# Kernel optimization log

Hardware: AMD Instinct MI355X
Metric: run time of the kernel (lower is better)

The kernel has to match this reference:

```python
import jax, jax.numpy as jnp
import numpy as np
import itertools

# ResamplerLayer(interpolation='LINEAR', boundary='REPLICATE'): trilinear
# resampling with replicate (clamp-to-edge) boundary handling.
# inputs: [B, X, Y, Z, C]; sample_coords: [B, D0, D1, D2, 3] in voxel units.

B, X, Y, Z, C = 2, 128, 128, 128, 4
D = 96  # output grid size per spatial dim


def setup_inputs() -> dict:
    key = jax.random.key(0)
    k1, k2 = jax.random.split(key)
    inputs = jax.random.normal(k1, (B, X, Y, Z, C), dtype=jnp.float32)
    sizes = jnp.array([X, Y, Z], dtype=jnp.float32)
    # coordinates in [-1, size] to exercise the replicate boundary slightly
    sample_coords = jax.random.uniform(k2, (B, D, D, D, 3), dtype=jnp.float32) * (sizes + 1.0) - 1.0
    return {"inputs": inputs, "sample_coords": sample_coords}


def _trilinear_replicate(inputs, sample_coords):
    spatial = inputs.shape[1:-1]          # (X, Y, Z)
    bsz = inputs.shape[0]
    floor_c = jnp.floor(sample_coords)
    w = sample_coords - floor_c           # fractional weights, [B, D0, D1, D2, 3]
    base = floor_c.astype(jnp.int32)
    # batch index broadcast against the spatial coord grid
    b_idx = jnp.arange(bsz).reshape((bsz,) + (1,) * (sample_coords.ndim - 2))
    out = jnp.zeros(sample_coords.shape[:-1] + (inputs.shape[-1],), dtype=inputs.dtype)
    for bits in itertools.product((0, 1), repeat=3):  # 8 corners (binary neighbour ids)
        ix = jnp.clip(base[..., 0] + bits[0], 0, spatial[0] - 1)  # REPLICATE boundary
        iy = jnp.clip(base[..., 1] + bits[1], 0, spatial[1] - 1)
        iz = jnp.clip(base[..., 2] + bits[2], 0, spatial[2] - 1)
        vals = inputs[b_idx, ix, iy, iz]  # gather: [B, D0, D1, D2, C]
        weight = jnp.ones(sample_coords.shape[:-1], dtype=inputs.dtype)
        for d, bit in enumerate(bits):
            weight = weight * (w[..., d] if bit else (1.0 - w[..., d]))
        out = out + vals * weight[..., None]
    return out


def reference(inputs, sample_coords):
    return _trilinear_replicate(inputs, sample_coords)
```

## Files before the change

kernel.cpp:

```cpp
#include <hip/hip_runtime.h>
#include <hip/hip_fp16.h>

#define BATCH 2
#define NS 128
#define NB 64
#define ND 96

constexpr int PPB   = ND * ND * ND;
constexpr int TOTAL = BATCH * PPB;
constexpr int BRICKS_PER_BATCH = NB * NB * NB;
constexpr int TOTAL_BRICKS = BATCH * BRICKS_PER_BATCH;
constexpr size_t WS_NEEDED = (size_t)TOTAL_BRICKS * 64;

__device__ __forceinline__ float4 f4_lerp(float4 a, float4 b, float t) {
    float4 r;
    r.x = fmaf(b.x - a.x, t, a.x);
    r.y = fmaf(b.y - a.y, t, a.y);
    r.z = fmaf(b.z - a.z, t, a.z);
    r.w = fmaf(b.w - a.w, t, a.w);
    return r;
}

__global__ __launch_bounds__(256) void repack_fp16_bricks(
    const float4* __restrict__ in, uint2* __restrict__ bricks)
{
    int g = blockIdx.x * 256 + threadIdx.x;
    int t = g >> 3;
    int l = g & 7;
    int lx = (l >> 2) & 1, ly = (l >> 1) & 1, lz = l & 1;
    int b  = t >> 18;
    int r  = t & 262143;
    int x  = ((r >> 12) << 1) + lx;
    int y  = (((r >> 6) & 63) << 1) + ly;
    int z  = ((r & 63) << 1) + lz;

    float4 v = in[(((size_t)b * NS + x) * NS + y) * NS + z];
    __half2 h0 = __float22half2_rn(make_float2(v.x, v.y));
    __half2 h1 = __float22half2_rn(make_float2(v.z, v.w));
    uint2 p;
    p.x = *(const unsigned int*)&h0;
    p.y = *(const unsigned int*)&h1;
    bricks[g] = p;
}

__device__ __forceinline__ float4 vox_to_f4(uint2 v) {
    __half2 a = *(const __half2*)&v.x;
    __half2 b = *(const __half2*)&v.y;
    float2 f0 = __half22float2(a);
    float2 f1 = __half22float2(b);
    return make_float4(f0.x, f0.y, f1.x, f1.y);
}

__device__ __forceinline__ int brick_off(int x, int y, int z) {
    int bidx = (((x >> 1) * NB) + (y >> 1)) * NB + (z >> 1);
    return (bidx << 3) + ((x & 1) << 2) + ((y & 1) << 1) + (z & 1);
}

__global__ __launch_bounds__(256) void resample_bricks(
    const uint2* __restrict__ bricks,
    const float* __restrict__ coords,
    float4*      __restrict__ out)
{
    int idx = blockIdx.x * 256 + threadIdx.x;
    if (idx >= TOTAL) return;

    const float cx = coords[3 * idx + 0];
    const float cy = coords[3 * idx + 1];
    const float cz = coords[3 * idx + 2];

    const float fx = floorf(cx), fy = floorf(cy), fz = floorf(cz);
    const float wx = cx - fx, wy = cy - fy, wz = cz - fz;

    int x0 = max(0, min((int)fx,     NS - 1));
    int x1 = max(0, min((int)fx + 1, NS - 1));
    int y0 = max(0, min((int)fy,     NS - 1));
    int y1 = max(0, min((int)fy + 1, NS - 1));
    int z0 = max(0, min((int)fz,     NS - 1));
    int z1 = max(0, min((int)fz + 1, NS - 1));

    const uint2* __restrict__ wb =
        bricks + ((idx >= PPB) ? (size_t)BRICKS_PER_BATCH * 8 : 0);

    uint2 u000 = wb[brick_off(x0, y0, z0)];
    uint2 u001 = wb[brick_off(x0, y0, z1)];
    uint2 u010 = wb[brick_off(x0, y1, z0)];
    uint2 u011 = wb[brick_off(x0, y1, z1)];
    uint2 u100 = wb[brick_off(x1, y0, z0)];
    uint2 u101 = wb[brick_off(x1, y0, z1)];
    uint2 u110 = wb[brick_off(x1, y1, z0)];
    uint2 u111 = wb[brick_off(x1, y1, z1)];

    float4 c00 = f4_lerp(vox_to_f4(u000), vox_to_f4(u001), wz);
    float4 c01 = f4_lerp(vox_to_f4(u010), vox_to_f4(u011), wz);
    float4 c10 = f4_lerp(vox_to_f4(u100), vox_to_f4(u101), wz);
    float4 c11 = f4_lerp(vox_to_f4(u110), vox_to_f4(u111), wz);

    float4 c0 = f4_lerp(c00, c01, wy);
    float4 c1 = f4_lerp(c10, c11, wy);
    out[idx] = f4_lerp(c0, c1, wx);
}

__global__ __launch_bounds__(256) void resample_direct(
    const float4* __restrict__ in,
    const float*  __restrict__ coords,
    float4*       __restrict__ out)
{
    int idx = blockIdx.x * blockDim.x + threadIdx.x;
    if (idx >= TOTAL) return;

    const float cx = coords[3 * idx + 0];
    const float cy = coords[3 * idx + 1];
    const float cz = coords[3 * idx + 2];
    const float fx = floorf(cx), fy = floorf(cy), fz = floorf(cz);
    const float wx = cx - fx, wy = cy - fy, wz = cz - fz;

    int x0 = max(0, min((int)fx,     NS - 1));
    int x1 = max(0, min((int)fx + 1, NS - 1));
    int y0 = max(0, min((int)fy,     NS - 1));
    int y1 = max(0, min((int)fy + 1, NS - 1));
    int z0 = max(0, min((int)fz,     NS - 1));
    int z1 = max(0, min((int)fz + 1, NS - 1));

    const int b = idx / PPB;
    const float4* __restrict__ inb = in + (size_t)b * (NS * NS * NS);
    const float4* r00 = inb + ((size_t)x0 * NS + y0) * NS;
    const float4* r01 = inb + ((size_t)x0 * NS + y1) * NS;
    const float4* r10 = inb + ((size_t)x1 * NS + y0) * NS;
    const float4* r11 = inb + ((size_t)x1 * NS + y1) * NS;

    float4 c00 = f4_lerp(r00[z0], r00[z1], wz);
    float4 c01 = f4_lerp(r01[z0], r01[z1], wz);
    float4 c10 = f4_lerp(r10[z0], r10[z1], wz);
    float4 c11 = f4_lerp(r11[z0], r11[z1], wz);
    float4 c0 = f4_lerp(c00, c01, wy);
    float4 c1 = f4_lerp(c10, c11, wy);
    out[idx] = f4_lerp(c0, c1, wx);
}

extern "C" void kernel_launch(void* const* d_in, const int* in_sizes, int n_in,
                              void* d_out, int out_size, void* d_ws, size_t ws_size,
                              hipStream_t stream) {
    const float4* in     = (const float4*)d_in[0];
    const float*  coords = (const float*)d_in[1];
    float4*       out    = (float4*)d_out;

    if (ws_size >= WS_NEEDED) {
        uint2* bricks = (uint2*)d_ws;
        int rp_threads = TOTAL_BRICKS * 8;
        repack_fp16_bricks<<<rp_threads / 256, 256, 0, stream>>>(in, bricks);
        resample_bricks<<<(TOTAL + 255) / 256, 256, 0, stream>>>(bricks, coords, out);
    } else {
        resample_direct<<<(TOTAL + 255) / 256, 256, 0, stream>>>(in, coords, out);
    }
}
```

Before: 195.4 us.

## Build fp16 yz-neighbour table so each sample needs two 32-byte loads

Adds a precompute kernel that stores, for every voxel, the four fp16 (y,z) neighbour corners in one 32-byte entry, laid out with x innermost. Each trilinear sample then needs two contiguous 32-byte reads instead of eight scattered 8-byte gathers. Each thread handles one point from each batch and writes outputs with nontemporal stores. The cost is a 4x redundant table (128 MB of workspace and a larger precompute write), and boundary weights are clamped by hand so the replicate padding stays correct.

```diff
diff --git a/kernel.cpp b/kernel.cpp
--- a/kernel.cpp
+++ b/kernel.cpp
@@ -10,7 +10,11 @@
 constexpr int TOTAL = BATCH * PPB;
 constexpr int BRICKS_PER_BATCH = NB * NB * NB;
 constexpr int TOTAL_BRICKS = BATCH * BRICKS_PER_BATCH;
-constexpr size_t WS_NEEDED = (size_t)TOTAL_BRICKS * 64;
+constexpr size_t WS_BRICKS = (size_t)TOTAL_BRICKS * 64;
+constexpr int ENTRIES_PER_BATCH = NS * NS * NS;
+constexpr size_t WS_R4 = (size_t)BATCH * ENTRIES_PER_BATCH * 32;
+
+typedef float fx4 __attribute__((ext_vector_type(4)));
 
 __device__ __forceinline__ float4 f4_lerp(float4 a, float4 b, float t) {
     float4 r;
@@ -21,8 +25,113 @@
     return r;
 }
 
+__device__ __forceinline__ uint2 pack_h4(float4 v) {
+    __half2 h0 = __float22half2_rn(make_float2(v.x, v.y));
+    __half2 h1 = __float22half2_rn(make_float2(v.z, v.w));
+    uint2 p;
+    p.x = *(const unsigned int*)&h0;
+    p.y = *(const unsigned int*)&h1;
+    return p;
+}
+
+__device__ __forceinline__ float4 unpack_h4(unsigned int a, unsigned int b) {
+    float2 f0 = __half22float2(*(const __half2*)&a);
+    float2 f1 = __half22float2(*(const __half2*)&b);
+    return make_float4(f0.x, f0.y, f1.x, f1.y);
+}
+
+__global__ __launch_bounds__(256) void build_r4_table(
+    const fx4* __restrict__ in, uint4* __restrict__ tab)
+{
+    int g = blockIdx.x * 256 + threadIdx.x;
+    int b = g >> 21;
+    int r = g & ((1 << 21) - 1);
+    int x = r & 127;
+    int z = (r >> 7) & 127;
+    int y = r >> 14;
+    int y1 = min(y + 1, NS - 1);
+    int z1 = min(z + 1, NS - 1);
+
+    const fx4* __restrict__ row = in + (((size_t)b * NS + x) * NS) * NS;
+    fx4 v00 = row[(size_t)y  * NS + z ];
+    fx4 v01 = row[(size_t)y  * NS + z1];
+    fx4 v10 = row[(size_t)y1 * NS + z ];
+    fx4 v11 = row[(size_t)y1 * NS + z1];
+
+    uint2 p00 = pack_h4(make_float4(v00.x, v00.y, v00.z, v00.w));
+    uint2 p01 = pack_h4(make_float4(v01.x, v01.y, v01.z, v01.w));
+    uint2 p10 = pack_h4(make_float4(v10.x, v10.y, v10.z, v10.w));
+    uint2 p11 = pack_h4(make_float4(v11.x, v11.y, v11.z, v11.w));
+
+    tab[2 * g + 0] = make_uint4(p00.x, p00.y, p01.x, p01.y);
+    tab[2 * g + 1] = make_uint4(p10.x, p10.y, p11.x, p11.y);
+}
+
+__device__ __forceinline__ float4 sample_r4(
+    const uint4* __restrict__ tb, float cx, float cy, float cz)
+{
+    const float fx = floorf(cx), fy = floorf(cy), fz = floorf(cz);
+    const float wx = cx - fx;
+    const float wy = (fy < 0.f) ? 0.f : (cy - fy);
+    const float wz = (fz < 0.f) ? 0.f : (cz - fz);
+
+    int x0 = max(0, min((int)fx,     NS - 1));
+    int x1 = max(0, min((int)fx + 1, NS - 1));
+    int y0 = max(0, min((int)fy,     NS - 1));
+    int z0 = max(0, min((int)fz,     NS - 1));
+
+    int ebase = ((y0 << 7) + z0) << 7;
+    const uint4* e0 = tb + 2 * (ebase + x0);
+    const uint4* e1 = tb + 2 * (ebase + x1);
+
+    uint4 lo0 = e0[0], hi0 = e0[1];
+    uint4 lo1 = e1[0], hi1 = e1[1];
+
+    float4 a00 = unpack_h4(lo0.x, lo0.y), a01 = unpack_h4(lo0.z, lo0.w);
+    float4 a10 = unpack_h4(hi0.x, hi0.y), a11 = unpack_h4(hi0.z, hi0.w);
+    float4 b00 = unpack_h4(lo1.x, lo1.y), b01 = unpack_h4(lo1.z, lo1.w);
+    float4 b10 = unpack_h4(hi1.x, hi1.y), b11 = unpack_h4(hi1.z, hi1.w);
+
+    float4 cA0 = f4_lerp(a00, a01, wz);
+    float4 cA1 = f4_lerp(a10, a11, wz);
+    float4 cB0 = f4_lerp(b00, b01, wz);
+    float4 cB1 = f4_lerp(b10, b11, wz);
+    float4 cA  = f4_lerp(cA0, cA1, wy);
+    float4 cB  = f4_lerp(cB0, cB1, wy);
+    return f4_lerp(cA, cB, wx);
+}
+
+__device__ __forceinline__ void nt_store4(float4 v, fx4* p) {
+    fx4 t; t.x = v.x; t.y = v.y; t.z = v.z; t.w = v.w;
+    __builtin_nontemporal_store(t, p);
+}
+
+__global__ __launch_bounds__(256) void resample_r4(
+    const uint4* __restrict__ tab,
+    const float* __restrict__ coords,
+    fx4*         __restrict__ out)
+{
+    int idx = blockIdx.x * 256 + threadIdx.x;
+    const int idxB = idx + PPB;
+
+    const float axc = coords[3 * idx + 0];
+    const float ayc = coords[3 * idx + 1];
+    const float azc = coords[3 * idx + 2];
+    const float bxc = coords[3 * idxB + 0];
+    const float byc = coords[3 * idxB + 1];
+    const float bzc = coords[3 * idxB + 2];
+
+    const uint4* tb0 = tab;
+    const uint4* tb1 = tab + (size_t)ENTRIES_PER_BATCH * 2;
+
+    float4 rA = sample_r4(tb0, axc, ayc, azc);
+    float4 rB = sample_r4(tb1, bxc, byc, bzc);
+    nt_store4(rA, &out[idx]);
+    nt_store4(rB, &out[idxB]);
+}
+
 __global__ __launch_bounds__(256) void repack_fp16_bricks(
-    const float4* __restrict__ in, uint2* __restrict__ bricks)
+    const fx4* __restrict__ in, uint2* __restrict__ bricks)
 {
     int g = blockIdx.x * 256 + threadIdx.x;
     int t = g >> 3;
@@ -34,21 +143,12 @@
     int y  = (((r >> 6) & 63) << 1) + ly;
     int z  = ((r & 63) << 1) + lz;
 
-    float4 v = in[(((size_t)b * NS + x) * NS + y) * NS + z];
-    __half2 h0 = __float22half2_rn(make_float2(v.x, v.y));
-    __half2 h1 = __float22half2_rn(make_float2(v.z, v.w));
-    uint2 p;
-    p.x = *(const unsigned int*)&h0;
-    p.y = *(const unsigned int*)&h1;
-    bricks[g] = p;
+    fx4 v = __builtin_nontemporal_load(&in[(((size_t)b * NS + x) * NS + y) * NS + z]);
+    bricks[g] = pack_h4(make_float4(v.x, v.y, v.z, v.w));
 }
 
 __device__ __forceinline__ float4 vox_to_f4(uint2 v) {
-    __half2 a = *(const __half2*)&v.x;
-    __half2 b = *(const __half2*)&v.y;
-    float2 f0 = __half22float2(a);
-    float2 f1 = __half22float2(b);
-    return make_float4(f0.x, f0.y, f1.x, f1.y);
+    return unpack_h4(v.x, v.y);
 }
 
 __device__ __forceinline__ int brick_off(int x, int y, int z) {
@@ -67,7 +167,6 @@
     const float cx = coords[3 * idx + 0];
     const float cy = coords[3 * idx + 1];
     const float cz = coords[3 * idx + 2];
-
     const float fx = floorf(cx), fy = floorf(cy), fz = floorf(cz);
     const float wx = cx - fx, wy = cy - fy, wz = cz - fz;
 
@@ -81,20 +180,15 @@
     const uint2* __restrict__ wb =
         bricks + ((idx >= PPB) ? (size_t)BRICKS_PER_BATCH * 8 : 0);
 
-    uint2 u000 = wb[brick_off(x0, y0, z0)];
-    uint2 u001 = wb[brick_off(x0, y0, z1)];
-    uint2 u010 = wb[brick_off(x0, y1, z0)];
-    uint2 u011 = wb[brick_off(x0, y1, z1)];
-    uint2 u100 = wb[brick_off(x1, y0, z0)];
-    uint2 u101 = wb[brick_off(x1, y0, z1)];
-    uint2 u110 = wb[brick_off(x1, y1, z0)];
-    uint2 u111 = wb[brick_off(x1, y1, z1)];
+    uint2 u000 = wb[brick_off(x0, y0, z0)], u001 = wb[brick_off(x0, y0, z1)];
+    uint2 u010 = wb[brick_off(x0, y1, z0)], u011 = wb[brick_off(x0, y1, z1)];
+    uint2 u100 = wb[brick_off(x1, y0, z0)], u101 = wb[brick_off(x1, y0, z1)];
+    uint2 u110 = wb[brick_off(x1, y1, z0)], u111 = wb[brick_off(x1, y1, z1)];
 
     float4 c00 = f4_lerp(vox_to_f4(u000), vox_to_f4(u001), wz);
     float4 c01 = f4_lerp(vox_to_f4(u010), vox_to_f4(u011), wz);
     float4 c10 = f4_lerp(vox_to_f4(u100), vox_to_f4(u101), wz);
     float4 c11 = f4_lerp(vox_to_f4(u110), vox_to_f4(u111), wz);
-
     float4 c0 = f4_lerp(c00, c01, wy);
     float4 c1 = f4_lerp(c10, c11, wy);
     out[idx] = f4_lerp(c0, c1, wx);
@@ -140,16 +234,20 @@
 extern "C" void kernel_launch(void* const* d_in, const int* in_sizes, int n_in,
                               void* d_out, int out_size, void* d_ws, size_t ws_size,
                               hipStream_t stream) {
-    const float4* in     = (const float4*)d_in[0];
-    const float*  coords = (const float*)d_in[1];
-    float4*       out    = (float4*)d_out;
-
-    if (ws_size >= WS_NEEDED) {
+    const float* coords = (const float*)d_in[1];
+
+    if (ws_size >= WS_R4) {
+        uint4* tab = (uint4*)d_ws;
+        int entries = BATCH * ENTRIES_PER_BATCH;
+        build_r4_table<<<entries / 256, 256, 0, stream>>>((const fx4*)d_in[0], tab);
+        resample_r4<<<PPB / 256, 256, 0, stream>>>(tab, coords, (fx4*)d_out);
+    } else if (ws_size >= WS_BRICKS) {
         uint2* bricks = (uint2*)d_ws;
         int rp_threads = TOTAL_BRICKS * 8;
-        repack_fp16_bricks<<<rp_threads / 256, 256, 0, stream>>>(in, bricks);
-        resample_bricks<<<(TOTAL + 255) / 256, 256, 0, stream>>>(bricks, coords, out);
+        repack_fp16_bricks<<<rp_threads / 256, 256, 0, stream>>>((const fx4*)d_in[0], bricks);
+        resample_bricks<<<(TOTAL + 255) / 256, 256, 0, stream>>>(bricks, coords, (float4*)d_out);
     } else {
-        resample_direct<<<(TOTAL + 255) / 256, 256, 0, stream>>>(in, coords, out);
+        resample_direct<<<(TOTAL + 255) / 256, 256, 0, stream>>>(
+            (const float4*)d_in[0], coords, (float4*)d_out);
     }
 }
```

New measurement: 247.4 us. 1.27x slower.
